# Optimization experiments

Hardware: AMD Instinct MI355X
Metric: run time of the kernel (lower is better)

The kernel has to match this reference:

```python
import jax, jax.numpy as jnp
import numpy as np

BLANK = 0
T, N, C, S = 1024, 64, 128, 128


def setup_inputs() -> dict:
    key = jax.random.key(0)
    k1, k2, k3, k4 = jax.random.split(key, 4)
    logits = jax.random.normal(k1, (T, N, C), dtype=jnp.float32)
    log_probs = jax.nn.log_softmax(logits, axis=-1)
    targets = jax.random.randint(k2, (N, S), 1, C).astype(jnp.int64)  # non-blank labels
    input_lengths = jax.random.randint(k3, (N,), T // 2, T + 1).astype(jnp.int32)
    target_lengths = jax.random.randint(k4, (N,), S // 2, S + 1).astype(jnp.int32)
    return {"log_probs": log_probs, "targets": targets,
            "input_lengths": input_lengths, "target_lengths": target_lengths}


def _ctc_loss(log_probs, targets, input_lengths, target_lengths):
    Tt, Nn, Cc = log_probs.shape
    Ss = targets.shape[1]
    Sx = 2 * Ss + 1  # extended target length (blanks interleaved)
    neg_inf = jnp.asarray(-jnp.inf, log_probs.dtype)

    ext = jnp.full((Nn, Sx), BLANK, dtype=jnp.int32).at[:, 1::2].set(targets.astype(jnp.int32))
    # emission log-prob of each extended state at each time: [T, N, Sx]
    emit = jnp.take_along_axis(log_probs, jnp.broadcast_to(ext[None], (Tt, Nn, Sx)), axis=2)
    # skip transition allowed when label[s] != label[s-2] (and s >= 2)
    skip = jnp.concatenate([jnp.zeros((Nn, 2), bool), ext[:, 2:] != ext[:, :-2]], axis=1)

    # faithful to the torch code: alphas initialized to ZEROS, then states 0,1 set
    alpha0 = jnp.zeros((Nn, Sx), log_probs.dtype)
    alpha0 = alpha0.at[:, 0].set(emit[0, :, 0]).at[:, 1].set(emit[0, :, 1])

    pad1 = jnp.full((Nn, 1), neg_inf, log_probs.dtype)
    pad2 = jnp.full((Nn, 2), neg_inf, log_probs.dtype)

    def step(alpha, emit_t):
        a_m1 = jnp.concatenate([pad1, alpha[:, :-1]], axis=1)
        a_m2 = jnp.where(skip, jnp.concatenate([pad2, alpha[:, :-2]], axis=1), neg_inf)
        new = jax.nn.logsumexp(jnp.stack([alpha, a_m1, a_m2]), axis=0) + emit_t
        return new, new

    _, rest = jax.lax.scan(step, alpha0, emit[1:])
    alphas = jnp.concatenate([alpha0[None], rest], axis=0)  # [T, N, Sx]

    n_idx = jnp.arange(Nn)
    v = alphas[input_lengths - 1, n_idx, 2 * target_lengths - 1]  # [N]
    # original: loss = -logsumexp over batch, then .mean() of a scalar (identity)
    return -jax.nn.logsumexp(v)


def reference(log_probs, targets, input_lengths, target_lengths):
    return _ctc_loss(log_probs, targets, input_lengths, target_lengths)
```

## Files before the change

### kernel.cpp

```cpp
#include <hip/hip_runtime.h>
#include <math.h>

#define TT 1024
#define NN 64
#define CC 128
#define SS 128
#define CH 32
#define NCHUNK 32
#define NC (NN * CC)

typedef float f4 __attribute__((ext_vector_type(4)));

#define DPP_QP_XOR1   0xB1
#define DPP_QP_XOR2   0x4E
#define DPP_WAVE_SHR1 0x138
#define DPP_ROW_MIRR  0x140
#define DPP_HALF_MIRR 0x141
#define DPP_BCAST15   0x142
#define DPP_BCAST31   0x143

template <int CTRL>
__device__ __forceinline__ float dpp_max_stage(float v) {
    int p = __builtin_amdgcn_update_dpp(__float_as_int(v), __float_as_int(v),
                                        CTRL, 0xF, 0xF, false);
    return fmaxf(v, __int_as_float(p));
}
__device__ __forceinline__ float dpp_shr1(float v) {
    int p = __builtin_amdgcn_update_dpp(0, __float_as_int(v),
                                        DPP_WAVE_SHR1, 0xF, 0xF, true);
    return __int_as_float(p);
}

#define DSR(dst, addr, off) \
    asm volatile("ds_read_b128 %0, %1 offset:" #off : "=v"(dst) : "v"(addr))
#define LGKM(n) do { \
    asm volatile("s_waitcnt lgkmcnt(" #n ")" ::: "memory"); \
    __builtin_amdgcn_sched_barrier(0); } while (0)
#define VMC(n) do { \
    asm volatile("s_waitcnt vmcnt(" #n ")" ::: "memory"); \
    __builtin_amdgcn_sched_barrier(0); } while (0)
#define ISSUE(mi, oea, oeb, opq) do { \
    DSR(gea[mi], base_e, oea); DSR(geb[mi], base_e, oeb); \
    DSR(gpq[mi], base_pq, opq); } while (0)
#define BARRIER() asm volatile("s_barrier" ::: "memory")

__global__ __launch_bounds__(256, 1) void ctc_scan(
    const float* __restrict__ lp,
    const int*   __restrict__ targets,
    const int*   __restrict__ ilen,
    const int*   __restrict__ tlen,
    float*       __restrict__ v_out)
{
    const int n    = blockIdx.x;
    const int tid  = threadIdx.x;
    const int wv   = tid >> 6;
    const int lane = tid & 63;

    __shared__ float  s_rows[2][CH][CC];
    __shared__ float4 s_e[2][CH / 2][64];
    __shared__ float4 s_pb4[2][CH / 4];

    const int tgA = targets[n * SS + 2 * lane];
    const int tgB = targets[n * SS + 2 * lane + 1];
    const float* lpn = lp + (size_t)n * CC;

    const int w = wv - 1;

    auto issue_rows = [&](int c, int buf) {
#pragma unroll
        for (int i = 0; i < 6; ++i) {
            const int idx = 3 * i + w;
            if (idx < 16) {
                const int r = 2 * idx;
                int t = 1 + c * CH + r + (lane >> 5);
                if (t > TT - 1) t = TT - 1;
                const float* src = lpn + (size_t)t * NC + (lane & 31) * 4;
                __builtin_amdgcn_global_load_lds(
                    (const __attribute__((address_space(1))) void*)src,
                    (__attribute__((address_space(3))) void*)&s_rows[buf][r][0],
                    16, 0, 0);
            }
        }
    };
    auto gather = [&](int buf, int ebuf) {
#pragma unroll
        for (int i = 0; i < 6; ++i) {
            const int k = 3 * i + w;
            if (k < 16) {
                const int rA = 2 * k, rB = rA + 1;
                const float pa0 = s_rows[buf][rA][tgA], pc0 = s_rows[buf][rA][tgB];
                const float pa1 = s_rows[buf][rB][tgA], pc1 = s_rows[buf][rB][tgB];
                s_e[ebuf][k][lane] =
                    make_float4(__expf(pa0), __expf(pc0), __expf(pa1), __expf(pc1));
            }
        }
        if (w == 2 && lane < CH) {
            const float pbv = s_rows[buf][lane][0];
            ((float*)s_pb4[ebuf])[lane] = __expf(pbv);
        }
    };

    if (wv != 0) {
        issue_rows(0, 0);
        issue_rows(1, 1);
        if (w == 0) { VMC(6); } else { VMC(5); }
        gather(0, 0);
    }

    const int tgBm = (lane > 0) ? targets[n * SS + 2 * lane - 1] : -1;
    const float k1f = (lane > 0 && tgA != tgBm) ? 1.f : 0.f;
    const float k3f = (tgB != tgA) ? 1.f : 0.f;
    const int il    = ilen[n];
    const int vs    = 2 * tlen[n] - 1;
    const int vlane = vs >> 2;

    float a0 = 1.f, a1 = 1.f, a2 = 1.f, a3 = 1.f, ls = 0.f;
    if (wv == 0) {
        a0 = (lane == 0) ? __expf(lpn[0])   : 1.f;
        a1 = (lane == 0) ? __expf(lpn[tgA]) : 1.f;
    }
    float a3p = (lane == 0) ? 0.f : 1.f;
    float mr = 1.f, inv = 1.f;

    const unsigned base_e0  = (unsigned)(size_t)(void*)&s_e[0][0][lane];
    const unsigned base_pq0 = (unsigned)(size_t)(void*)&s_pb4[0][0];

    __syncthreads();

    if (wv == 0) __builtin_amdgcn_s_setprio(1);

    for (int cc = 0; cc < NCHUNK; ++cc) {
        const int b = cc & 1;
        if (wv == 0) {
            const int t0 = 1 + cc * CH;
            const bool cap = ((unsigned)(il - 1 - t0) < (unsigned)CH);
            const unsigned base_e  = base_e0  + (unsigned)(b << 14);
            const unsigned base_pq = base_pq0 + (unsigned)(b << 7);

            f4 gea[3], geb[3], gpq[3];

            auto group4 = [&](const f4& ea, const f4& eb, const f4& pq, int jbase) {
#pragma unroll
                for (int c = 0; c < 4; ++c) {
                    const int j = jbase + c;
                    const float cpa = (c==0)?ea[0]:(c==1)?ea[2]:(c==2)?eb[0]:eb[2];
                    const float cpc = (c==0)?ea[1]:(c==1)?ea[3]:(c==2)?eb[1]:eb[3];
                    const float cpb = pq[c];

                    float nb3 = fmaf(k3f, a1, a3 + a2) * cpc;
                    float a3pn = dpp_shr1(nb3);
                    float nb0 = (a0 + a3p) * cpb;
                    float nb1 = fmaf(k1f, a3p, a0 + a1) * cpa;
                    float nb2 = (a2 + a1) * cpb;

                    const int jj = j & 7;
                    if      (jj == 0) mr = fmaxf(fmaxf(nb0, nb1), fmaxf(nb2, nb3));
                    else if (jj == 1) mr = dpp_max_stage<DPP_QP_XOR1>(mr);
                    else if (jj == 2) mr = dpp_max_stage<DPP_QP_XOR2>(mr);
                    else if (jj == 3) mr = dpp_max_stage<DPP_HALF_MIRR>(mr);
                    else if (jj == 4) mr = dpp_max_stage<DPP_ROW_MIRR>(mr);
                    else if (jj == 5) mr = dpp_max_stage<DPP_BCAST15>(mr);
                    else if (jj == 6) mr = dpp_max_stage<DPP_BCAST31>(mr);
                    else {
                        const float mru = __int_as_float(
                            __builtin_amdgcn_readlane(__float_as_int(mr), 63));
                        inv = 1.0f / mru;
                        ls += __logf(mru);
                        nb0 *= inv; nb1 *= inv; nb2 *= inv; nb3 *= inv;
                    }

                    if (cap) {
                        const int t = t0 + j;
                        if (t == il - 1 && lane == vlane)
                            v_out[n] = __logf((vs & 2) ? nb3 : nb1) + ls;
                    }

                    a0 = nb0; a1 = nb1; a2 = nb2; a3 = nb3;
                    if (jj == 7) a3pn *= inv;
                    a3p = a3pn;
                }
            };

            ISSUE(0, 0,     1024,  0);
            ISSUE(1, 2048,  3072,  16);
            ISSUE(2, 4096,  5120,  32);  LGKM(6); group4(gea[0], geb[0], gpq[0], 0);
            ISSUE(0, 6144,  7168,  48);  LGKM(6); group4(gea[1], geb[1], gpq[1], 4);
            ISSUE(1, 8192,  9216,  64);  LGKM(6); group4(gea[2], geb[2], gpq[2], 8);
            ISSUE(2, 10240, 11264, 80);  LGKM(6); group4(gea[0], geb[0], gpq[0], 12);
            ISSUE(0, 12288, 13312, 96);  LGKM(6); group4(gea[1], geb[1], gpq[1], 16);
            ISSUE(1, 14336, 15360, 112); LGKM(6); group4(gea[2], geb[2], gpq[2], 20);
                                         LGKM(3); group4(gea[0], geb[0], gpq[0], 24);
                                         LGKM(0); group4(gea[1], geb[1], gpq[1], 28);
        } else {
            issue_rows(cc + 2, cc & 1);
            if (w == 0) { VMC(6); } else { VMC(5); }
            if (cc + 1 < NCHUNK) gather((cc + 1) & 1, (cc + 1) & 1);
            asm volatile("s_waitcnt lgkmcnt(0)" ::: "memory");
        }
        BARRIER();
    }
}

__global__ void ctc_reduce(const float* __restrict__ v, float* __restrict__ out)
{
    const int lane = threadIdx.x;
    float x = v[lane];
    float m = x;
#pragma unroll
    for (int off = 32; off > 0; off >>= 1) m = fmaxf(m, __shfl_xor(m, off));
    float e = __expf(x - m);
#pragma unroll
    for (int off = 32; off > 0; off >>= 1) e += __shfl_xor(e, off);
    if (lane == 0) out[0] = -(m + __logf(e));
}

extern "C" void kernel_launch(void* const* d_in, const int* in_sizes, int n_in,
                              void* d_out, int out_size, void* d_ws, size_t ws_size,
                              hipStream_t stream) {
    const float* lp      = (const float*)d_in[0];
    const int*   targets = (const int*)d_in[1];
    const int*   ilen    = (const int*)d_in[2];
    const int*   tlen    = (const int*)d_in[3];

    float* v   = (float*)d_ws;
    float* out = (float*)d_out;

    ctc_scan<<<NN, 256, 0, stream>>>(lp, targets, ilen, tlen, v);
    ctc_reduce<<<1, 64, 0, stream>>>(v, out);
}
```

Before: 72.01 us.

## Precompute exp emissions in a separate kernel and scan with a single-wave ring buffer

Adds a fully parallel pre-pass that gathers and exponentiates the blank and label emission probabilities for every (t, n) into a workspace array. The scan then runs as one 64-thread wave per sequence and streams the precomputed emissions through an LDS ring using async global-to-LDS loads. This removes the in-scan gather, the producer/consumer warp split and the per-chunk barriers. In exchange it writes and re-reads a large intermediate buffer of roughly 64 MB and adds a kernel launch. The old kernel stays as a fallback when the workspace is too small.

```diff
diff --git a/kernel.cpp b/kernel.cpp
--- a/kernel.cpp
+++ b/kernel.cpp
@@ -39,12 +39,146 @@
 #define VMC(n) do { \
     asm volatile("s_waitcnt vmcnt(" #n ")" ::: "memory"); \
     __builtin_amdgcn_sched_barrier(0); } while (0)
-#define ISSUE(mi, oea, oeb, opq) do { \
-    DSR(gea[mi], base_e, oea); DSR(geb[mi], base_e, oeb); \
-    DSR(gpq[mi], base_pq, opq); } while (0)
 #define BARRIER() asm volatile("s_barrier" ::: "memory")
 
-__global__ __launch_bounds__(256, 1) void ctc_scan(
+__global__ __launch_bounds__(256) void ctc_emit(
+    const float* __restrict__ lp,
+    const int*   __restrict__ targets,
+    float4*      __restrict__ E)
+{
+    const int wid  = blockIdx.x * 4 + (threadIdx.x >> 6);
+    const int lane = threadIdx.x & 63;
+    const int t = wid & (TT - 1);
+    const int n = wid >> 10;
+
+    const float* row = lp + ((size_t)t * NN + n) * CC;
+    const int tgA = targets[n * SS + 2 * lane];
+    const int tgB = targets[n * SS + 2 * lane + 1];
+
+    const float pb = __expf(row[0]);
+    const float pa = __expf(row[tgA]);
+    const float pc = __expf(row[tgB]);
+    E[(((size_t)n << 10) + t) * 64 + lane] = make_float4(pb, pa, pc, 0.f);
+}
+
+__global__ __launch_bounds__(64) void ctc_scan_lone(
+    const float4* __restrict__ E,
+    const int*    __restrict__ targets,
+    const int*    __restrict__ ilen,
+    const int*    __restrict__ tlen,
+    float*        __restrict__ v_out)
+{
+    const int n    = blockIdx.x;
+    const int lane = threadIdx.x;
+
+    __shared__ float4 ring[16][4][64];
+
+    const int tgA  = targets[n * SS + 2 * lane];
+    const int tgB  = targets[n * SS + 2 * lane + 1];
+    const int tgBm = (lane > 0) ? targets[n * SS + 2 * lane - 1] : -1;
+    const float k1f = (lane > 0 && tgA != tgBm) ? 1.f : 0.f;
+    const float k3f = (tgB != tgA) ? 1.f : 0.f;
+
+    const int il    = ilen[n];
+    const int vs    = 2 * tlen[n] - 1;
+    const int vlane = vs >> 2;
+
+    const float4* En = E + (((size_t)n) << 10) * 64;
+
+    VMC(0);
+
+#pragma unroll
+    for (int g = 0; g < 8; ++g) {
+#pragma unroll
+        for (int c = 0; c < 4; ++c) {
+            const float* src = (const float*)(En + (size_t)(4 * g + c) * 64) + lane * 4;
+            __builtin_amdgcn_global_load_lds(
+                (const __attribute__((address_space(1))) void*)src,
+                (__attribute__((address_space(3))) void*)&ring[g][c][0],
+                16, 0, 0);
+        }
+    }
+
+    float a0 = 1.f, a1 = 1.f, a2 = 1.f, a3 = 1.f, ls = 0.f;
+    float a3p = (lane == 0) ? 0.f : 1.f;
+    float mr = 1.f, inv = 1.f;
+
+    for (int og = 0; og < 32; ++og) {
+        const int wh = ((og + 1) & 1) << 3;
+        const int rh = (og & 1) << 3;
+#pragma unroll
+        for (int i = 0; i < 8; ++i) {
+            const int g   = og * 8 + i;
+            const int t0g = 4 * g;
+            VMC(28);
+
+            const float4 e0 = ring[rh + i][0][lane];
+            const float4 e1 = ring[rh + i][1][lane];
+            const float4 e2 = ring[rh + i][2][lane];
+            const float4 e3 = ring[rh + i][3][lane];
+
+            {
+                int gn = g + 8; if (gn > 255) gn = 255;
+#pragma unroll
+                for (int c = 0; c < 4; ++c) {
+                    const float* src =
+                        (const float*)(En + (size_t)(4 * gn + c) * 64) + lane * 4;
+                    __builtin_amdgcn_global_load_lds(
+                        (const __attribute__((address_space(1))) void*)src,
+                        (__attribute__((address_space(3))) void*)&ring[wh + i][c][0],
+                        16, 0, 0);
+                }
+                __builtin_amdgcn_sched_barrier(0);
+            }
+
+            const bool cap = ((unsigned)(il - 1 - t0g) < 4u);
+#pragma unroll
+            for (int c = 0; c < 4; ++c) {
+                const int t = t0g + c;
+                const float4 e = (c == 0) ? e0 : (c == 1) ? e1 : (c == 2) ? e2 : e3;
+                if (g == 0 && c == 0) {
+                    a0 = (lane == 0) ? e.x : 1.f;
+                    a1 = (lane == 0) ? e.y : 1.f;
+                    continue;
+                }
+                const float cpb = e.x, cpa = e.y, cpc = e.z;
+
+                float nb3 = fmaf(k3f, a1, a3 + a2) * cpc;
+                float a3pn = dpp_shr1(nb3);
+                float nb0 = (a0 + a3p) * cpb;
+                float nb1 = fmaf(k1f, a3p, a0 + a1) * cpa;
+                float nb2 = (a2 + a1) * cpb;
+
+                const int jj = (i & 1) * 4 + c;
+                if      (jj == 0) mr = fmaxf(fmaxf(nb0, nb1), fmaxf(nb2, nb3));
+                else if (jj == 1) mr = dpp_max_stage<DPP_QP_XOR1>(mr);
+                else if (jj == 2) mr = dpp_max_stage<DPP_QP_XOR2>(mr);
+                else if (jj == 3) mr = dpp_max_stage<DPP_HALF_MIRR>(mr);
+                else if (jj == 4) mr = dpp_max_stage<DPP_ROW_MIRR>(mr);
+                else if (jj == 5) mr = dpp_max_stage<DPP_BCAST15>(mr);
+                else if (jj == 6) mr = dpp_max_stage<DPP_BCAST31>(mr);
+                else {
+                    const float mru = __int_as_float(
+                        __builtin_amdgcn_readlane(__float_as_int(mr), 63));
+                    inv = 1.0f / mru;
+                    ls += __logf(mru);
+                    nb0 *= inv; nb1 *= inv; nb2 *= inv; nb3 *= inv;
+                }
+
+                if (cap) {
+                    if (t == il - 1 && lane == vlane)
+                        v_out[n] = __logf((vs & 2) ? nb3 : nb1) + ls;
+                }
+
+                a0 = nb0; a1 = nb1; a2 = nb2; a3 = nb3;
+                if (jj == 7) a3pn *= inv;
+                a3p = a3pn;
+            }
+        }
+    }
+}
+
+__global__ __launch_bounds__(256, 1) void ctc_scan_fb(
     const float* __restrict__ lp,
     const int*   __restrict__ targets,
     const int*   __restrict__ ilen,
@@ -63,7 +197,6 @@
     const int tgA = targets[n * SS + 2 * lane];
     const int tgB = targets[n * SS + 2 * lane + 1];
     const float* lpn = lp + (size_t)n * CC;
-
     const int w = wv - 1;
 
     auto issue_rows = [&](int c, int buf) {
@@ -126,7 +259,6 @@
     const unsigned base_pq0 = (unsigned)(size_t)(void*)&s_pb4[0][0];
 
     __syncthreads();
-
     if (wv == 0) __builtin_amdgcn_s_setprio(1);
 
     for (int cc = 0; cc < NCHUNK; ++cc) {
@@ -138,13 +270,16 @@
             const unsigned base_pq = base_pq0 + (unsigned)(b << 7);
 
             f4 gea[3], geb[3], gpq[3];
-
-            auto group4 = [&](const f4& ea, const f4& eb, const f4& pq, int jbase) {
+#define ISSUE(mi, oea, oeb, opq) do { \
+    DSR(gea[mi], base_e, oea); DSR(geb[mi], base_e, oeb); \
+    DSR(gpq[mi], base_pq, opq); } while (0)
+
+            auto group4 = [&](const f4& ea, const f4& eb2, const f4& pq, int jbase) {
 #pragma unroll
                 for (int c = 0; c < 4; ++c) {
                     const int j = jbase + c;
-                    const float cpa = (c==0)?ea[0]:(c==1)?ea[2]:(c==2)?eb[0]:eb[2];
-                    const float cpc = (c==0)?ea[1]:(c==1)?ea[3]:(c==2)?eb[1]:eb[3];
+                    const float cpa = (c==0)?ea[0]:(c==1)?ea[2]:(c==2)?eb2[0]:eb2[2];
+                    const float cpc = (c==0)?ea[1]:(c==1)?ea[3]:(c==2)?eb2[1]:eb2[3];
                     const float cpb = pq[c];
 
                     float nb3 = fmaf(k3f, a1, a3 + a2) * cpc;
@@ -191,6 +326,7 @@
             ISSUE(1, 14336, 15360, 112); LGKM(6); group4(gea[2], geb[2], gpq[2], 20);
                                          LGKM(3); group4(gea[0], geb[0], gpq[0], 24);
                                          LGKM(0); group4(gea[1], geb[1], gpq[1], 28);
+#undef ISSUE
         } else {
             issue_rows(cc + 2, cc & 1);
             if (w == 0) { VMC(6); } else { VMC(5); }
@@ -225,6 +361,13 @@
     float* v   = (float*)d_ws;
     float* out = (float*)d_out;
 
-    ctc_scan<<<NN, 256, 0, stream>>>(lp, targets, ilen, tlen, v);
+    const size_t NEED = 256 + (size_t)TT * NN * 64 * sizeof(float4);
+    if (ws_size >= NEED) {
+        float4* E = (float4*)((char*)d_ws + 256);
+        ctc_emit<<<TT * NN / 4, 256, 0, stream>>>(lp, targets, E);
+        ctc_scan_lone<<<NN, 64, 0, stream>>>(E, targets, ilen, tlen, v);
+    } else {
+        ctc_scan_fb<<<NN, 256, 0, stream>>>(lp, targets, ilen, tlen, v);
+    }
     ctc_reduce<<<1, 64, 0, stream>>>(v, out);
 }
```

New measurement: 103.4 us. 43.6% more time.
